# Kernel optimization log

Measured on AMD Instinct MI355X. Metric: run time of the kernel, lower is better.

Reference implementation:

```python
import jax, jax.numpy as jnp
import numpy as np

B = 512       # batch
D = 256       # n_embd
NH = 4        # heads
NN = 8 * D // NH   # neurons per head = 512
NTOT = NH * NN     # 2048
DH = D // NH       # 64
K = 8              # thinking steps
EPS_LN = 1e-5


def _ln(x, g, b):
    mu = jnp.mean(x, axis=-1, keepdims=True)
    var = jnp.mean((x - mu) ** 2, axis=-1, keepdims=True)
    return (x - mu) * jax.lax.rsqrt(var + EPS_LN) * g + b


def setup_inputs() -> dict:
    key = jax.random.key(0)
    ks = jax.random.split(key, 12)
    s = 0.02
    w = lambda k, shape: (jax.random.normal(k, shape, jnp.float32) * s)
    return {
        "boards": jax.random.normal(ks[0], (B, 12, 8, 8), jnp.float32),
        # board_encoder: Linear(768,d) -> GELU -> LN(d) -> Linear(d,d); weights stored (in,out)
        "enc_w1": w(ks[1], (768, D)), "enc_b1": jnp.zeros((D,), jnp.float32),
        "enc_ln_g": jnp.ones((D,), jnp.float32), "enc_ln_b": jnp.zeros((D,), jnp.float32),
        "enc_w2": w(ks[2], (D, D)), "enc_b2": jnp.zeros((D,), jnp.float32),
        "xinit_w": w(ks[3], (D, NTOT)), "xinit_b": jnp.zeros((NTOT,), jnp.float32),
        "D_y": w(ks[4], (NH, D, NN)),
        "E": w(ks[5], (NTOT, D)),
        "D_x": w(ks[6], (NH, D, NN)),
        "By_w": w(ks[7], (D, D)),
        "Bx_w": w(ks[8], (D, D)),
        "lna_g": jnp.ones((D,), jnp.float32), "lna_b": jnp.zeros((D,), jnp.float32),
        "lnz_g": jnp.ones((D,), jnp.float32), "lnz_b": jnp.zeros((D,), jnp.float32),
        "log_damping": jnp.asarray(np.log(0.9 / 0.1), jnp.float32),
        "vh_w1": w(ks[9], (D, D // 2)), "vh_b1": jnp.zeros((D // 2,), jnp.float32),
        "vh_w2": w(ks[10], (D // 2, 1)), "vh_b2": jnp.zeros((1,), jnp.float32),
    }


def reference(boards, enc_w1, enc_b1, enc_ln_g, enc_ln_b, enc_w2, enc_b2,
              xinit_w, xinit_b, D_y, E, D_x, By_w, Bx_w,
              lna_g, lna_b, lnz_g, lnz_b, log_damping,
              vh_w1, vh_b1, vh_w2, vh_b2):
    Bn = boards.shape[0]
    flat = boards.reshape(Bn, 768)
    h = jax.nn.gelu(flat @ enc_w1 + enc_b1, approximate=False)
    h = _ln(h, enc_ln_g, enc_ln_b)
    b = h @ enc_w2 + enc_b2                      # (B, d)
    x0 = jax.nn.relu(b @ xinit_w + xinit_b)      # (B, n)
    rho0 = jnp.zeros((Bn, NH, NN, DH), boards.dtype)
    lam = jax.nn.sigmoid(log_damping)
    b_y = b @ By_w
    b_x = b @ Bx_w

    def step(carry, _):
        x, rho = carry
        x_h = x.reshape(Bn, NH, NN)
        a = jnp.einsum('bhnd,bhn->bhd', rho, x_h).reshape(Bn, D)   # read from scratchpad
        a_cond = _ln(a + b_y, lna_g, lna_b)
        g = jax.nn.relu(jnp.einsum('bd,hdn->bhn', a_cond, D_y))
        y = (g * x_h).reshape(Bn, NTOT)
        z = _ln(y @ E, lnz_g, lnz_b)
        dx = jax.nn.relu(jnp.einsum('bd,hdn->bhn', z + b_x, D_x))
        x_new = x + dx.reshape(Bn, NTOT)
        xh = x_new.reshape(Bn, NH, NN)
        x_write = xh / (jnp.linalg.norm(xh, axis=-1, keepdims=True) + 1e-8)
        z_h = z.reshape(Bn, NH, DH)
        rho_new = lam * rho + (1.0 - lam) * jnp.einsum('bhn,bhd->bhnd', x_write, z_h)
        return (x_new, rho_new), z

    (_, _), zs = jax.lax.scan(step, (x0, rho0), None, length=K)
    z_last = zs[-1]                              # (B, d) from final thinking step
    v = jnp.tanh(jax.nn.gelu(z_last @ vh_w1 + vh_b1, approximate=False) @ vh_w2 + vh_b2)
    return v                                     # (B, 1)
```

## Files before the change

### kernel.cpp

```cpp
#include <hip/hip_runtime.h>
#include <hip/hip_bf16.h>
#include <math.h>

#define B_ 512
#define D_ 256
#define NH_ 4
#define NN_ 512
#define NTOT_ 2048
#define DH_ 64
#define KSTEPS 8

typedef __attribute__((ext_vector_type(8))) short bf16x8;
typedef __attribute__((ext_vector_type(4))) float f32x4;

#if __has_builtin(__builtin_amdgcn_global_load_lds)
#define HAVE_GLL 1
#else
#define HAVE_GLL 0
#endif

__device__ __forceinline__ float gelu_exact(float x) {
  return 0.5f * x * (1.0f + erff(x * 0.70710678118654752f));
}

__device__ __forceinline__ unsigned short f2b(float f) {
  union { float f; unsigned int u; } x; x.f = f;
  unsigned int u = x.u;
  unsigned int r = (u + 0x7FFFu + ((u >> 16) & 1u)) >> 16;
  return (unsigned short)r;
}

__device__ __forceinline__ float blockReduceSum256(float v, float* red) {
  int t = threadIdx.x;
  red[t] = v; __syncthreads();
  #pragma unroll
  for (int st = 128; st > 0; st >>= 1) {
    if (t < st) red[t] += red[t + st];
    __syncthreads();
  }
  float r = red[0];
  __syncthreads();
  return r;
}

#if HAVE_GLL
__device__ __forceinline__ void load16_lds(const unsigned short* g, unsigned short* l) {
  __builtin_amdgcn_global_load_lds(
      (const __attribute__((address_space(1))) unsigned int*)g,
      (__attribute__((address_space(3))) unsigned int*)l, 16, 0, 0);
}
#endif

template<int EPI>
__global__ __launch_bounds__(512) void k_gemm_x(
    const unsigned short* __restrict__ A, const unsigned short* __restrict__ W,
    const float* __restrict__ bias, float* __restrict__ xio)
{
  __shared__ __align__(16) unsigned short As[2 * 4096];
  __shared__ __align__(16) unsigned short Ws[2 * 4096];
  const int t = threadIdx.x;
  const int lane = t & 63, w = t >> 6;
  const int lr = lane & 15, lk = lane >> 4;
  const int l3 = lane >> 3, cch = lane & 7;
  const int n0 = blockIdx.x * 64, m0 = blockIdx.y * 64;
  const int wm = w & 3, wn = w >> 2;

  f32x4 acc[2];
  acc[0] = (f32x4){0.f, 0.f, 0.f, 0.f};
  acc[1] = (f32x4){0.f, 0.f, 0.f, 0.f};

#if HAVE_GLL
  #define STGX(tt) {                                                              \
      int buf_ = (tt) & 1; int kk_ = (tt) * 64;                                   \
      int r_ = w * 8 + l3;                                                        \
      load16_lds(&A[(size_t)(m0 + r_) * 256 + kk_ + ((cch ^ (r_ & 7)) << 3)],     \
                 &As[buf_ * 4096 + w * 512]);                                     \
      load16_lds(&W[(size_t)(n0 + r_) * 256 + kk_ + ((cch ^ (r_ & 7)) << 3)],     \
                 &Ws[buf_ * 4096 + w * 512]); }
  STGX(0);
  for (int tt = 0; tt < 4; tt++) {
    asm volatile("s_waitcnt vmcnt(0)" ::: "memory");
    __builtin_amdgcn_s_barrier();
    asm volatile("" ::: "memory");
    if (tt + 1 < 4) STGX(tt + 1);
    const unsigned short* Ab = &As[(tt & 1) * 4096];
    const unsigned short* Wb = &Ws[(tt & 1) * 4096];
    #pragma unroll
    for (int ks = 0; ks < 2; ks++) {
      int q = ks * 4 + lk;
      int r = wm * 16 + lr;
      bf16x8 af = *(const bf16x8*)&Ab[r * 64 + ((q ^ (r & 7)) << 3)];
      #pragma unroll
      for (int j = 0; j < 2; j++) {
        int c = wn * 32 + j * 16 + lr;
        bf16x8 bf = *(const bf16x8*)&Wb[c * 64 + ((q ^ (c & 7)) << 3)];
        acc[j] = __builtin_amdgcn_mfma_f32_16x16x32_bf16(af, bf, acc[j], 0, 0, 0);
      }
    }
  }
  #undef STGX
#else
  for (int tt = 0; tt < 4; tt++) {
    int buf_ = tt & 1; int kk_ = tt * 64;
    int r_ = w * 8 + l3;
    bf16x8 va = *(const bf16x8*)&A[(size_t)(m0 + r_) * 256 + kk_ + ((cch ^ (r_ & 7)) << 3)];
    *(bf16x8*)&As[buf_ * 4096 + r_ * 64 + cch * 8] = va;
    bf16x8 vw = *(const bf16x8*)&W[(size_t)(n0 + r_) * 256 + kk_ + ((cch ^ (r_ & 7)) << 3)];
    *(bf16x8*)&Ws[buf_ * 4096 + r_ * 64 + cch * 8] = vw;
    __syncthreads();
    const unsigned short* Ab = &As[buf_ * 4096];
    const unsigned short* Wb = &Ws[buf_ * 4096];
    #pragma unroll
    for (int ks = 0; ks < 2; ks++) {
      int q = ks * 4 + lk;
      int r = wm * 16 + lr;
      bf16x8 af = *(const bf16x8*)&Ab[r * 64 + ((q ^ (r & 7)) << 3)];
      #pragma unroll
      for (int j = 0; j < 2; j++) {
        int c = wn * 32 + j * 16 + lr;
        bf16x8 bf = *(const bf16x8*)&Wb[c * 64 + ((q ^ (c & 7)) << 3)];
        acc[j] = __builtin_amdgcn_mfma_f32_16x16x32_bf16(af, bf, acc[j], 0, 0, 0);
      }
    }
    __syncthreads();
  }
#endif

  #pragma unroll
  for (int j = 0; j < 2; j++)
    #pragma unroll
    for (int qq = 0; qq < 4; qq++) {
      int r = m0 + wm * 16 + lk * 4 + qq;
      int c = n0 + wn * 32 + j * 16 + lr;
      float v = acc[j][qq];
      if (EPI == 0) v = fmaxf(v + bias[c], 0.f);
      else          v = fmaxf(v, 0.f) + xio[(size_t)r * NTOT_ + c];
      xio[(size_t)r * NTOT_ + c] = v;
    }
}

__global__ __launch_bounds__(512) void k_yz(
    const unsigned short* __restrict__ acond_bf, const unsigned short* __restrict__ DyT,
    const unsigned short* __restrict__ ET, const float* __restrict__ x,
    float* __restrict__ zparts)
{
  __shared__ __align__(16) unsigned short As[2 * 4096];
  __shared__ __align__(16) unsigned short Ws[2 * 4096];
  __shared__ __align__(16) unsigned short Es[256 * 64];
  __shared__ __align__(16) unsigned short ytile[64 * 64];
  const int t = threadIdx.x;
  const int lane = t & 63, w = t >> 6;
  const int lr = lane & 15, lk = lane >> 4;
  const int l3 = lane >> 3, cch = lane & 7;
  const int nt_ = blockIdx.x, mt = blockIdx.y;
  const int m0 = mt * 64, n0 = nt_ * 64;
  const int wm = w & 3, wn = w >> 2;

  f32x4 acc[2];
  acc[0] = (f32x4){0.f, 0.f, 0.f, 0.f};
  acc[1] = (f32x4){0.f, 0.f, 0.f, 0.f};

#if HAVE_GLL
  #define STGY(tt) {                                                                  \
      int buf_ = (tt) & 1; int kk_ = (tt) * 64;                                       \
      int r_ = w * 8 + l3;                                                            \
      load16_lds(&acond_bf[(size_t)(m0 + r_) * 256 + kk_ + ((cch ^ (r_ & 7)) << 3)],  \
                 &As[buf_ * 4096 + w * 512]);                                         \
      load16_lds(&DyT[(size_t)(n0 + r_) * 256 + kk_ + ((cch ^ (r_ & 7)) << 3)],       \
                 &Ws[buf_ * 4096 + w * 512]); }
  STGY(0);
  #pragma unroll
  for (int p = 0; p < 4; p++) {
    int d = p * 64 + w * 8 + l3;
    load16_lds(&ET[(size_t)d * 2048 + n0 + ((cch ^ (d & 7)) << 3)],
               &Es[(p * 64 + w * 8) * 64]);
  }
  for (int tt = 0; tt < 4; tt++) {
    asm volatile("s_waitcnt vmcnt(0)" ::: "memory");
    __builtin_amdgcn_s_barrier();
    asm volatile("" ::: "memory");
    if (tt + 1 < 4) STGY(tt + 1);
    const unsigned short* Ab = &As[(tt & 1) * 4096];
    const unsigned short* Wb = &Ws[(tt & 1) * 4096];
    #pragma unroll
    for (int ks = 0; ks < 2; ks++) {
      int q = ks * 4 + lk;
      int r = wm * 16 + lr;
      bf16x8 af = *(const bf16x8*)&Ab[r * 64 + ((q ^ (r & 7)) << 3)];
      #pragma unroll
      for (int j = 0; j < 2; j++) {
        int c = wn * 32 + j * 16 + lr;
        bf16x8 bf = *(const bf16x8*)&Wb[c * 64 + ((q ^ (c & 7)) << 3)];
        acc[j] = __builtin_amdgcn_mfma_f32_16x16x32_bf16(af, bf, acc[j], 0, 0, 0);
      }
    }
  }
  #undef STGY
#else
  #pragma unroll
  for (int p = 0; p < 4; p++) {
    int d = p * 64 + w * 8 + l3;
    bf16x8 ve = *(const bf16x8*)&ET[(size_t)d * 2048 + n0 + ((cch ^ (d & 7)) << 3)];
    *(bf16x8*)&Es[d * 64 + cch * 8] = ve;
  }
  for (int tt = 0; tt < 4; tt++) {
    int buf_ = tt & 1; int kk_ = tt * 64;
    int r_ = w * 8 + l3;
    bf16x8 va = *(const bf16x8*)&acond_bf[(size_t)(m0 + r_) * 256 + kk_ + ((cch ^ (r_ & 7)) << 3)];
    *(bf16x8*)&As[buf_ * 4096 + r_ * 64 + cch * 8] = va;
    bf16x8 vw = *(const bf16x8*)&DyT[(size_t)(n0 + r_) * 256 + kk_ + ((cch ^ (r_ & 7)) << 3)];
    *(bf16x8*)&Ws[buf_ * 4096 + r_ * 64 + cch * 8] = vw;
    __syncthreads();
    const unsigned short* Ab = &As[buf_ * 4096];
    const unsigned short* Wb = &Ws[buf_ * 4096];
    #pragma unroll
    for (int ks = 0; ks < 2; ks++) {
      int q = ks * 4 + lk;
      int r = wm * 16 + lr;
      bf16x8 af = *(const bf16x8*)&Ab[r * 64 + ((q ^ (r & 7)) << 3)];
      #pragma unroll
      for (int j = 0; j < 2; j++) {
        int c = wn * 32 + j * 16 + lr;
        bf16x8 bf = *(const bf16x8*)&Wb[c * 64 + ((q ^ (c & 7)) << 3)];
        acc[j] = __builtin_amdgcn_mfma_f32_16x16x32_bf16(af, bf, acc[j], 0, 0, 0);
      }
    }
    __syncthreads();
  }
#endif

  #pragma unroll
  for (int j = 0; j < 2; j++)
    #pragma unroll
    for (int qq = 0; qq < 4; qq++) {
      int rl = wm * 16 + lk * 4 + qq;
      int cl = wn * 32 + j * 16 + lr;
      float v = fmaxf(acc[j][qq], 0.f) * x[(size_t)(m0 + rl) * NTOT_ + n0 + cl];
      ytile[rl * 64 + ((((cl >> 3) ^ (rl & 7)) << 3) | (cl & 7))] = f2b(v);
    }
  __syncthreads();

  f32x4 zacc[8];
  #pragma unroll
  for (int j = 0; j < 8; j++) zacc[j] = (f32x4){0.f, 0.f, 0.f, 0.f};
  #pragma unroll
  for (int ks = 0; ks < 2; ks++) {
    int q = ks * 4 + lk;
    int r = wm * 16 + lr;
    bf16x8 af = *(const bf16x8*)&ytile[r * 64 + ((q ^ (r & 7)) << 3)];
    #pragma unroll
    for (int j = 0; j < 8; j++) {
      int c = wn * 128 + j * 16 + lr;
      bf16x8 bf = *(const bf16x8*)&Es[c * 64 + ((q ^ (c & 7)) << 3)];
      zacc[j] = __builtin_amdgcn_mfma_f32_16x16x32_bf16(af, bf, zacc[j], 0, 0, 0);
    }
  }
  float* zp = zparts + (size_t)nt_ * (B_ * D_);
  #pragma unroll
  for (int j = 0; j < 8; j++)
    #pragma unroll
    for (int qq = 0; qq < 4; qq++) {
      int r = m0 + wm * 16 + lk * 4 + qq;
      int d = wn * 128 + j * 16 + lr;
      zp[(size_t)r * D_ + d] = zacc[j][qq];
    }
}

template<int ACT>
__global__ __launch_bounds__(256) void gemm_tile(
    const float* __restrict__ A, const float* __restrict__ W,
    const float* __restrict__ bias, float* __restrict__ out,
    unsigned short* __restrict__ outb, int M, int N, int K, int kchunk)
{
  __shared__ float As[16][68];
  __shared__ float Bs[16][68];
  const int tid = threadIdx.x;
  const int row0 = blockIdx.y * 64;
  const int col0 = blockIdx.x * 64;
  const int k0 = blockIdx.z * kchunk;
  const int ty = tid >> 4, tx = tid & 15;
  const int ar = tid >> 4, ak = tid & 15;
  const int br = tid >> 6, bc = tid & 63;
  float acc[4][4] = {};
  for (int kk = k0; kk < k0 + kchunk; kk += 16) {
    #pragma unroll
    for (int i = 0; i < 4; i++) {
      int r = ar + i * 16;
      As[ak][r] = A[(size_t)(row0 + r) * K + kk + ak];
    }
    #pragma unroll
    for (int i = 0; i < 4; i++) {
      int kr = br + i * 4;
      Bs[kr][bc] = W[(size_t)(kk + kr) * N + col0 + bc];
    }
    __syncthreads();
    #pragma unroll
    for (int q = 0; q < 16; q++) {
      float4 av = *(const float4*)&As[q][ty * 4];
      float4 bv = *(const float4*)&Bs[q][tx * 4];
      float aa[4] = {av.x, av.y, av.z, av.w};
      float bb[4] = {bv.x, bv.y, bv.z, bv.w};
      #pragma unroll
      for (int i = 0; i < 4; i++)
        #pragma unroll
        for (int j = 0; j < 4; j++)
          acc[i][j] = fmaf(aa[i], bb[j], acc[i][j]);
    }
    __syncthreads();
  }
  const bool parts = (gridDim.z > 1);
  float* o = out + (parts ? (size_t)blockIdx.z * (size_t)M * N : (size_t)0);
  #pragma unroll
  for (int i = 0; i < 4; i++) {
    int r = row0 + ty * 4 + i;
    #pragma unroll
    for (int j = 0; j < 4; j++) {
      int c = col0 + tx * 4 + j;
      float v = acc[i][j];
      if (!parts) {
        if (bias) v += bias[c];
        if (ACT == 2) v = gelu_exact(v);
      }
      o[(size_t)r * N + c] = v;
      if (!parts && outb) outb[(size_t)r * N + c] = f2b(v);
    }
  }
}

__global__ __launch_bounds__(256) void k_prep(
    const float* __restrict__ D_y, const float* __restrict__ D_x,
    const float* __restrict__ xinit_w, const float* __restrict__ E,
    const float* __restrict__ By_w, const float* __restrict__ Bx_w,
    unsigned short* __restrict__ DyT, unsigned short* __restrict__ DxT,
    unsigned short* __restrict__ xinitT, unsigned short* __restrict__ ET,
    float* __restrict__ Wcat)
{
  const int t = threadIdx.x;
  if (blockIdx.y == 4) {
    if (blockIdx.x >= 32) return;
    int k0 = ((int)blockIdx.x >> 3) * 64, n0 = ((int)blockIdx.x & 7) * 64;
    for (int i = 0; i < 16; i++) {
      int local = i * 256 + t;
      int kk = local >> 6, nn = local & 63;
      int n = n0 + nn;
      float v = (n < 256) ? By_w[(size_t)(k0 + kk) * 256 + n]
                          : Bx_w[(size_t)(k0 + kk) * 256 + (n - 256)];
      Wcat[(size_t)(k0 + kk) * 512 + n] = v;
    }
    return;
  }
  __shared__ float T[64][65];
  const float* in; unsigned short* out; int Kd, Nd, head, nx;
  switch (blockIdx.y) {
    case 0:  in = D_y;     out = DyT;    Kd = 256;  Nd = 2048; head = 1; nx = 32; break;
    case 1:  in = D_x;     out = DxT;    Kd = 256;  Nd = 2048; head = 1; nx = 32; break;
    case 2:  in = xinit_w; out = xinitT; Kd = 256;  Nd = 2048; head = 0; nx = 32; break;
    default: in = E;       out = ET;     Kd = 2048; Nd = 256;  head = 0; nx = 4;  break;
  }
  const int n0 = ((int)blockIdx.x % nx) * 64, k0 = ((int)blockIdx.x / nx) * 64;
  const int tx = t & 63, ty = t >> 6;
  #pragma unroll
  for (int i = 0; i < 16; i++) {
    int k = k0 + ty + i * 4;
    int n = n0 + tx;
    float v;
    if (head) v = in[((size_t)(n >> 9) * 256 + k) * 512 + (n & 511)];
    else      v = in[(size_t)k * Nd + n];
    T[ty + i * 4][tx] = v;
  }
  __syncthreads();
  #pragma unroll
  for (int i = 0; i < 16; i++) {
    int n = n0 + ty + i * 4;
    out[(size_t)n * Kd + k0 + tx] = f2b(T[tx][ty + i * 4]);
  }
}

__global__ __launch_bounds__(256) void k_ln_enc(
    const float* __restrict__ in, int nparts, int stride,
    const float* __restrict__ pre_bias,
    const float* __restrict__ g, const float* __restrict__ bta,
    float* __restrict__ out)
{
  __shared__ float red[256];
  int b = blockIdx.x, d = threadIdx.x;
  float v = 0.f;
  for (int p = 0; p < nparts; p++) v += in[(size_t)p * stride + (size_t)b * 256 + d];
  v = gelu_exact(v + pre_bias[d]);
  float mu = blockReduceSum256(v, red) * (1.f / 256.f);
  float c = v - mu;
  float var = blockReduceSum256(c * c, red) * (1.f / 256.f);
  out[(size_t)b * 256 + d] = c * rsqrtf(var + 1e-5f) * g[d] + bta[d];
}

template<int VAL>
__global__ __launch_bounds__(256) void k_ln_z(
    const float* __restrict__ zparts, const float* __restrict__ bybx,
    const float* __restrict__ lnz_g, const float* __restrict__ lnz_b,
    float* __restrict__ zh_k, unsigned short* __restrict__ zbx_bf,
    const float* __restrict__ w1, const float* __restrict__ b1,
    const float* __restrict__ w2, const float* __restrict__ b2,
    float* __restrict__ vout)
{
  __shared__ float red[256];
  __shared__ float zn[256];
  int b = blockIdx.x, d = threadIdx.x;
  float v = 0.f;
  #pragma unroll
  for (int p = 0; p < 32; p++) v += zparts[(size_t)p * (B_ * D_) + (size_t)b * D_ + d];
  float mu = blockReduceSum256(v, red) * (1.f / 256.f);
  float c = v - mu;
  float var = blockReduceSum256(c * c, red) * (1.f / 256.f);
  float vn = c * rsqrtf(var + 1e-5f) * lnz_g[d] + lnz_b[d];
  zh_k[(size_t)b * D_ + d] = vn;
  zbx_bf[(size_t)b * D_ + d] = f2b(vn + bybx[(size_t)b * 512 + 256 + d]);
  if (VAL) {
    zn[d] = vn; __syncthreads();
    int j = d & 127, ih = d >> 7;
    float s = 0.f;
    #pragma unroll 4
    for (int i = ih * 128; i < ih * 128 + 128; i++) s += zn[i] * w1[(size_t)i * 128 + j];
    red[d] = s; __syncthreads();
    if (d < 128) red[d] = gelu_exact(red[d] + red[d + 128] + b1[j]) * w2[d];
    __syncthreads();
    #pragma unroll
    for (int st = 64; st > 0; st >>= 1) {
      if (d < st) red[d] += red[d + st];
      __syncthreads();
    }
    if (d == 0) vout[b] = tanhf(red[0] + b2[0]);
  }
}

__global__ __launch_bounds__(256) void k_step_a(
    const float* __restrict__ x, float* __restrict__ xw_hist,
    const float* __restrict__ z_hist, const float* __restrict__ bybx,
    const float* __restrict__ lna_g, const float* __restrict__ lna_b,
    const float* __restrict__ log_damp, int k, unsigned short* __restrict__ out)
{
  __shared__ float dots[KSTEPS][NH_];
  __shared__ float red[256];
  int b = blockIdx.x, t = threadIdx.x;
  int lane = t & 63, wv = t >> 6;
  float lam = 1.f / (1.f + expf(-log_damp[0]));
  const float* xb = x + (size_t)b * NTOT_;
  float xv[8];
  #pragma unroll
  for (int i = 0; i < 8; i++) xv[i] = xb[t * 8 + i];

  if (k >= 1) {
    float s = 0.f;
    #pragma unroll
    for (int i = 0; i < 8; i++) s += xv[i] * xv[i];
    #pragma unroll
    for (int m = 1; m < 64; m <<= 1) s += __shfl_xor(s, m, 64);
    float inv = 1.f / (sqrtf(s) + 1e-8f);
    float* xwo = xw_hist + ((size_t)(k - 1) * B_ + b) * NTOT_;
    #pragma unroll
    for (int i = 0; i < 8; i++) xwo[t * 8 + i] = xv[i] * inv;
    if (lane == 0) dots[k - 1][wv] = s * inv;
  }
  for (int j = 0; j < k - 1; j++) {
    const float* xwb = xw_hist + ((size_t)j * B_ + b) * NTOT_;
    float s = 0.f;
    #pragma unroll
    for (int i = 0; i < 8; i++) s += xv[i] * xwb[t * 8 + i];
    #pragma unroll
    for (int off = 32; off > 0; off >>= 1) s += __shfl_down(s, off, 64);
    if (lane == 0) dots[j][wv] = s;
  }
  __syncthreads();

  int d = t;
  float av = 0.f, lp = 1.f;
  for (int j = k - 1; j >= 0; j--) {
    av += (1.f - lam) * lp * dots[j][d >> 6] * z_hist[((size_t)j * B_ + b) * D_ + d];
    lp *= lam;
  }
  av += bybx[(size_t)b * 512 + d];
  float mu = blockReduceSum256(av, red) * (1.f / 256.f);
  float c = av - mu;
  float var = blockReduceSum256(c * c, red) * (1.f / 256.f);
  out[(size_t)b * D_ + d] = f2b(c * rsqrtf(var + 1e-5f) * lna_g[d] + lna_b[d]);
}

extern "C" void kernel_launch(void* const* d_in, const int* in_sizes, int n_in,
                              void* d_out, int out_size, void* d_ws, size_t ws_size,
                              hipStream_t stream) {
  const float* boards   = (const float*)d_in[0];
  const float* enc_w1   = (const float*)d_in[1];
  const float* enc_b1   = (const float*)d_in[2];
  const float* enc_ln_g = (const float*)d_in[3];
  const float* enc_ln_b = (const float*)d_in[4];
  const float* enc_w2   = (const float*)d_in[5];
  const float* enc_b2   = (const float*)d_in[6];
  const float* xinit_w  = (const float*)d_in[7];
  const float* xinit_b  = (const float*)d_in[8];
  const float* D_y      = (const float*)d_in[9];
  const float* E        = (const float*)d_in[10];
  const float* D_x      = (const float*)d_in[11];
  const float* By_w     = (const float*)d_in[12];
  const float* Bx_w     = (const float*)d_in[13];
  const float* lna_g    = (const float*)d_in[14];
  const float* lna_b    = (const float*)d_in[15];
  const float* lnz_g    = (const float*)d_in[16];
  const float* lnz_b    = (const float*)d_in[17];
  const float* log_damp = (const float*)d_in[18];
  const float* vh_w1    = (const float*)d_in[19];
  const float* vh_b1    = (const float*)d_in[20];
  const float* vh_w2    = (const float*)d_in[21];
  const float* vh_b2    = (const float*)d_in[22];
  float* outp = (float*)d_out;

  float* ws = (float*)d_ws;
  size_t o = 0;
  float* x      = ws + o; o += (size_t)B_ * NTOT_;
  float* xw     = ws + o; o += (size_t)KSTEPS * B_ * NTOT_;
  float* zh     = ws + o; o += (size_t)KSTEPS * B_ * D_;
  float* hparts = ws + o; o += (size_t)8 * B_ * D_;
  float* h      = ws + o; o += (size_t)B_ * D_;
  float* bvec   = ws + o; o += (size_t)B_ * D_;
  float* bybx   = ws + o; o += (size_t)B_ * 512;
  float* Wcat   = ws + o; o += (size_t)256 * 512;
  float* zparts = ws + o; o += (size_t)32 * B_ * D_;
  unsigned short* DyT     = (unsigned short*)(ws + o); o += (size_t)NTOT_ * D_ / 2;
  unsigned short* DxT     = (unsigned short*)(ws + o); o += (size_t)NTOT_ * D_ / 2;
  unsigned short* ET      = (unsigned short*)(ws + o); o += (size_t)D_ * NTOT_ / 2;
  unsigned short* xinitT  = (unsigned short*)(ws + o); o += (size_t)NTOT_ * D_ / 2;
  unsigned short* bvec_bf = (unsigned short*)(ws + o); o += (size_t)B_ * D_ / 2;
  unsigned short* acond_bf= (unsigned short*)(ws + o); o += (size_t)B_ * D_ / 2;
  unsigned short* zbx_bf  = (unsigned short*)(ws + o); o += (size_t)B_ * D_ / 2;

  k_prep<<<dim3(128, 5), 256, 0, stream>>>(D_y, D_x, xinit_w, E, By_w, Bx_w,
                                           DyT, DxT, xinitT, ET, Wcat);
  gemm_tile<0><<<dim3(4, 8, 8), 256, 0, stream>>>(boards, enc_w1, nullptr, hparts,
                                                  nullptr, B_, D_, 768, 96);
  k_ln_enc<<<B_, 256, 0, stream>>>(hparts, 8, B_ * D_, enc_b1, enc_ln_g, enc_ln_b, h);
  gemm_tile<0><<<dim3(4, 8, 1), 256, 0, stream>>>(h, enc_w2, enc_b2, bvec, bvec_bf,
                                                  B_, D_, D_, D_);
  gemm_tile<0><<<dim3(8, 8, 1), 256, 0, stream>>>(bvec, Wcat, nullptr, bybx, nullptr,
                                                  B_, 512, D_, D_);
  k_gemm_x<0><<<dim3(32, 8), 512, 0, stream>>>(bvec_bf, xinitT, xinit_b, x);

  for (int k = 0; k < KSTEPS; k++) {
    k_step_a<<<B_, 256, 0, stream>>>(x, xw, zh, bybx, lna_g, lna_b, log_damp, k, acond_bf);
    k_yz<<<dim3(32, 8), 512, 0, stream>>>(acond_bf, DyT, ET, x, zparts);
    if (k < KSTEPS - 1) {
      k_ln_z<0><<<B_, 256, 0, stream>>>(zparts, bybx, lnz_g, lnz_b,
                                        zh + (size_t)k * B_ * D_, zbx_bf,
                                        nullptr, nullptr, nullptr, nullptr, nullptr);
      k_gemm_x<1><<<dim3(32, 8), 512, 0, stream>>>(zbx_bf, DxT, nullptr, x);
    } else {
      k_ln_z<1><<<B_, 256, 0, stream>>>(zparts, bybx, lnz_g, lnz_b,
                                        zh + (size_t)k * B_ * D_, zbx_bf,
                                        vh_w1, vh_b1, vh_w2, vh_b2, outp);
    }
  }
}
```

Baseline: 389.0 us.

## Fuse scratchpad read and LayerNorm into k_yz, compute dots in gemm_x epilogue

Removes the per-step k_step_a kernel. The x·xw history dot products and per-head norms are now accumulated with atomics in the k_gemm_x epilogue, and k_yz rebuilds a_cond (decayed sum of z history plus b_y, then LayerNorm) directly into LDS before the D_y GEMM. k_yz also writes the normalized xw rows and zeroes the double-buffered dot and norm buffers. This saves one launch per step and the acond_bf round trip through global memory. In exchange it adds atomics, redundant a_cond computation in every n-tile block (32x), and extra LDS use.

```diff
diff --git a/kernel.cpp b/kernel.cpp
--- a/kernel.cpp
+++ b/kernel.cpp
@@ -4,10 +4,7 @@
 
 #define B_ 512
 #define D_ 256
-#define NH_ 4
-#define NN_ 512
 #define NTOT_ 2048
-#define DH_ 64
 #define KSTEPS 8
 
 typedef __attribute__((ext_vector_type(8))) short bf16x8;
@@ -43,18 +40,34 @@
   return r;
 }
 
+__device__ __forceinline__ float red8(float v) {
+  v += __shfl_xor(v, 1, 64); v += __shfl_xor(v, 2, 64); v += __shfl_xor(v, 4, 64);
+  return v;
+}
+
 #if HAVE_GLL
-__device__ __forceinline__ void load16_lds(const unsigned short* g, unsigned short* l) {
+__device__ __forceinline__ void stage16(const unsigned short* g, unsigned short* base, int lane) {
+  (void)lane;
   __builtin_amdgcn_global_load_lds(
       (const __attribute__((address_space(1))) unsigned int*)g,
-      (__attribute__((address_space(3))) unsigned int*)l, 16, 0, 0);
-}
+      (__attribute__((address_space(3))) unsigned int*)base, 16, 0, 0);
+}
+#define WAITV0 asm volatile("s_waitcnt vmcnt(0)" ::: "memory")
+#else
+__device__ __forceinline__ void stage16(const unsigned short* g, unsigned short* base, int lane) {
+  *(bf16x8*)(base + lane * 8) = *(const bf16x8*)g;
+}
+#define WAITV0 asm volatile("s_waitcnt vmcnt(0) lgkmcnt(0)" ::: "memory")
 #endif
 
-template<int EPI>
+#define BAR() { __builtin_amdgcn_s_barrier(); asm volatile("" ::: "memory"); }
+
+template<int EPI, int DOTS>
 __global__ __launch_bounds__(512) void k_gemm_x(
     const unsigned short* __restrict__ A, const unsigned short* __restrict__ W,
-    const float* __restrict__ bias, float* __restrict__ xio)
+    const float* __restrict__ bias, float* __restrict__ xio,
+    const float* __restrict__ xw, float* __restrict__ dotbuf,
+    float* __restrict__ normbuf, int k)
 {
   __shared__ __align__(16) unsigned short As[2 * 4096];
   __shared__ __align__(16) unsigned short Ws[2 * 4096];
@@ -69,19 +82,17 @@
   acc[0] = (f32x4){0.f, 0.f, 0.f, 0.f};
   acc[1] = (f32x4){0.f, 0.f, 0.f, 0.f};
 
-#if HAVE_GLL
   #define STGX(tt) {                                                              \
       int buf_ = (tt) & 1; int kk_ = (tt) * 64;                                   \
       int r_ = w * 8 + l3;                                                        \
-      load16_lds(&A[(size_t)(m0 + r_) * 256 + kk_ + ((cch ^ (r_ & 7)) << 3)],     \
-                 &As[buf_ * 4096 + w * 512]);                                     \
-      load16_lds(&W[(size_t)(n0 + r_) * 256 + kk_ + ((cch ^ (r_ & 7)) << 3)],     \
-                 &Ws[buf_ * 4096 + w * 512]); }
+      stage16(&A[(size_t)(m0 + r_) * 256 + kk_ + ((cch ^ (r_ & 7)) << 3)],        \
+              &As[buf_ * 4096 + w * 512], lane);                                  \
+      stage16(&W[(size_t)(n0 + r_) * 256 + kk_ + ((cch ^ (r_ & 7)) << 3)],        \
+              &Ws[buf_ * 4096 + w * 512], lane); }
   STGX(0);
   for (int tt = 0; tt < 4; tt++) {
-    asm volatile("s_waitcnt vmcnt(0)" ::: "memory");
-    __builtin_amdgcn_s_barrier();
-    asm volatile("" ::: "memory");
+    WAITV0;
+    BAR();
     if (tt + 1 < 4) STGX(tt + 1);
     const unsigned short* Ab = &As[(tt & 1) * 4096];
     const unsigned short* Wb = &Ws[(tt & 1) * 4096];
@@ -97,35 +108,11 @@
         acc[j] = __builtin_amdgcn_mfma_f32_16x16x32_bf16(af, bf, acc[j], 0, 0, 0);
       }
     }
+    BAR();
   }
   #undef STGX
-#else
-  for (int tt = 0; tt < 4; tt++) {
-    int buf_ = tt & 1; int kk_ = tt * 64;
-    int r_ = w * 8 + l3;
-    bf16x8 va = *(const bf16x8*)&A[(size_t)(m0 + r_) * 256 + kk_ + ((cch ^ (r_ & 7)) << 3)];
-    *(bf16x8*)&As[buf_ * 4096 + r_ * 64 + cch * 8] = va;
-    bf16x8 vw = *(const bf16x8*)&W[(size_t)(n0 + r_) * 256 + kk_ + ((cch ^ (r_ & 7)) << 3)];
-    *(bf16x8*)&Ws[buf_ * 4096 + r_ * 64 + cch * 8] = vw;
-    __syncthreads();
-    const unsigned short* Ab = &As[buf_ * 4096];
-    const unsigned short* Wb = &Ws[buf_ * 4096];
-    #pragma unroll
-    for (int ks = 0; ks < 2; ks++) {
-      int q = ks * 4 + lk;
-      int r = wm * 16 + lr;
-      bf16x8 af = *(const bf16x8*)&Ab[r * 64 + ((q ^ (r & 7)) << 3)];
-      #pragma unroll
-      for (int j = 0; j < 2; j++) {
-        int c = wn * 32 + j * 16 + lr;
-        bf16x8 bf = *(const bf16x8*)&Wb[c * 64 + ((q ^ (c & 7)) << 3)];
-        acc[j] = __builtin_amdgcn_mfma_f32_16x16x32_bf16(af, bf, acc[j], 0, 0, 0);
-      }
-    }
-    __syncthreads();
-  }
-#endif
-
+
+  float vout[2][4];
   #pragma unroll
   for (int j = 0; j < 2; j++)
     #pragma unroll
@@ -136,107 +123,176 @@
       if (EPI == 0) v = fmaxf(v + bias[c], 0.f);
       else          v = fmaxf(v, 0.f) + xio[(size_t)r * NTOT_ + c];
       xio[(size_t)r * NTOT_ + c] = v;
-    }
+      vout[j][qq] = v;
+    }
+
+  if (DOTS) {
+    __syncthreads();
+    float* xfl = (float*)&As[0];
+    #pragma unroll
+    for (int j = 0; j < 2; j++)
+      #pragma unroll
+      for (int qq = 0; qq < 4; qq++)
+        xfl[(wm * 16 + lk * 4 + qq) * 64 + wn * 32 + j * 16 + lr] = vout[j][qq];
+    __syncthreads();
+    const int row = t >> 3, sub = t & 7;
+    const int gr = m0 + row;
+    const int headx = n0 >> 9;
+    const int p = k & 1;
+    float xv8[8]; float nrm = 0.f;
+    #pragma unroll
+    for (int e = 0; e < 8; e++) {
+      xv8[e] = xfl[row * 64 + sub * 8 + e];
+      nrm += xv8[e] * xv8[e];
+    }
+    nrm = red8(nrm);
+    if (sub == 0) atomicAdd(&normbuf[(p * 512 + gr) * 4 + headx], nrm);
+    for (int j = 0; j < k; j++) {
+      const float* wr = &xw[((size_t)j * B_ + gr) * NTOT_ + n0 + sub * 8];
+      float s = 0.f;
+      #pragma unroll
+      for (int e = 0; e < 8; e++) s += xv8[e] * wr[e];
+      s = red8(s);
+      if (sub == 0) atomicAdd(&dotbuf[((p * 7 + j) * 512 + gr) * 4 + headx], s);
+    }
+  }
 }
 
 __global__ __launch_bounds__(512) void k_yz(
-    const unsigned short* __restrict__ acond_bf, const unsigned short* __restrict__ DyT,
-    const unsigned short* __restrict__ ET, const float* __restrict__ x,
-    float* __restrict__ zparts)
+    const unsigned short* __restrict__ DyT, const unsigned short* __restrict__ ET,
+    const float* __restrict__ x, const float* __restrict__ bybx,
+    const float* __restrict__ zhg,
+    const float* __restrict__ lna_g, const float* __restrict__ lna_b,
+    const float* __restrict__ log_damp,
+    float* __restrict__ xw, float* __restrict__ dotbuf, float* __restrict__ normbuf,
+    float* __restrict__ zparts, int k)
 {
-  __shared__ __align__(16) unsigned short As[2 * 4096];
-  __shared__ __align__(16) unsigned short Ws[2 * 4096];
+  __shared__ __align__(16) unsigned short Abuf[4][4096];
+  __shared__ __align__(16) unsigned short Dys[4][4096];
   __shared__ __align__(16) unsigned short Es[256 * 64];
-  __shared__ __align__(16) unsigned short ytile[64 * 64];
+  __shared__ __align__(16) unsigned short ytile[4096];
+  __shared__ float invn_s[64];
   const int t = threadIdx.x;
   const int lane = t & 63, w = t >> 6;
   const int lr = lane & 15, lk = lane >> 4;
   const int l3 = lane >> 3, cch = lane & 7;
-  const int nt_ = blockIdx.x, mt = blockIdx.y;
-  const int m0 = mt * 64, n0 = nt_ * 64;
+  const int nt = blockIdx.x, mt = blockIdx.y;
+  const int m0 = mt * 64, n0 = nt * 64;
   const int wm = w & 3, wn = w >> 2;
-
-  f32x4 acc[2];
-  acc[0] = (f32x4){0.f, 0.f, 0.f, 0.f};
-  acc[1] = (f32x4){0.f, 0.f, 0.f, 0.f};
-
-#if HAVE_GLL
-  #define STGY(tt) {                                                                  \
-      int buf_ = (tt) & 1; int kk_ = (tt) * 64;                                       \
-      int r_ = w * 8 + l3;                                                            \
-      load16_lds(&acond_bf[(size_t)(m0 + r_) * 256 + kk_ + ((cch ^ (r_ & 7)) << 3)],  \
-                 &As[buf_ * 4096 + w * 512]);                                         \
-      load16_lds(&DyT[(size_t)(n0 + r_) * 256 + kk_ + ((cch ^ (r_ & 7)) << 3)],       \
-                 &Ws[buf_ * 4096 + w * 512]); }
-  STGY(0);
+  const int qb = (k - 1) & 1, pz = k & 1;
+
+  #pragma unroll
+  for (int kt = 0; kt < 4; kt++) {
+    int rr = w * 8 + l3;
+    stage16(&DyT[(size_t)(n0 + rr) * 256 + kt * 64 + ((cch ^ (rr & 7)) << 3)],
+            &Dys[kt][w * 512], lane);
+  }
   #pragma unroll
   for (int p = 0; p < 4; p++) {
     int d = p * 64 + w * 8 + l3;
-    load16_lds(&ET[(size_t)d * 2048 + n0 + ((cch ^ (d & 7)) << 3)],
-               &Es[(p * 64 + w * 8) * 64]);
-  }
-  for (int tt = 0; tt < 4; tt++) {
-    asm volatile("s_waitcnt vmcnt(0)" ::: "memory");
-    __builtin_amdgcn_s_barrier();
-    asm volatile("" ::: "memory");
-    if (tt + 1 < 4) STGY(tt + 1);
-    const unsigned short* Ab = &As[(tt & 1) * 4096];
-    const unsigned short* Wb = &Ws[(tt & 1) * 4096];
+    stage16(&ET[(size_t)d * 2048 + n0 + ((cch ^ (d & 7)) << 3)],
+            &Es[(p * 64 + w * 8) * 64], lane);
+  }
+
+  {
+    const float lam = 1.f / (1.f + expf(-log_damp[0]));
+    const int row = t >> 3, sub = t & 7;
+    const int gr = m0 + row;
+    const int head = sub >> 1;
+    float a8[32];
+    #pragma unroll
+    for (int i = 0; i < 32; i++) a8[i] = 0.f;
+    if (k >= 1) {
+      float nb = normbuf[(qb * 512 + gr) * 4 + head];
+      if (sub == 0) {
+        float nx = normbuf[(qb * 512 + gr) * 4 + (n0 >> 9)];
+        invn_s[row] = 1.f / (sqrtf(nx) + 1e-8f);
+      }
+      float lp = 1.f;
+      for (int j = k - 1; j >= 0; j--) {
+        float djv = (j == k - 1) ? nb / (sqrtf(nb) + 1e-8f)
+                                 : dotbuf[((qb * 7 + j) * 512 + gr) * 4 + head];
+        float cj = (1.f - lam) * lp * djv;
+        const float* zr = zhg + ((size_t)j * B_ + gr) * D_ + sub * 32;
+        #pragma unroll
+        for (int i8 = 0; i8 < 8; i8++) {
+          float4 zv = *(const float4*)(zr + i8 * 4);
+          a8[i8 * 4 + 0] += cj * zv.x; a8[i8 * 4 + 1] += cj * zv.y;
+          a8[i8 * 4 + 2] += cj * zv.z; a8[i8 * 4 + 3] += cj * zv.w;
+        }
+        lp *= lam;
+      }
+    }
+    const float* byr = bybx + (size_t)gr * 512 + sub * 32;
+    #pragma unroll
+    for (int i8 = 0; i8 < 8; i8++) {
+      float4 bv = *(const float4*)(byr + i8 * 4);
+      a8[i8 * 4 + 0] += bv.x; a8[i8 * 4 + 1] += bv.y;
+      a8[i8 * 4 + 2] += bv.z; a8[i8 * 4 + 3] += bv.w;
+    }
+    float s = 0.f;
+    #pragma unroll
+    for (int i = 0; i < 32; i++) s += a8[i];
+    s = red8(s);
+    float mu = s * (1.f / 256.f);
+    float s2 = 0.f;
+    #pragma unroll
+    for (int i = 0; i < 32; i++) { float cc = a8[i] - mu; s2 += cc * cc; }
+    s2 = red8(s2);
+    float rin = rsqrtf(s2 * (1.f / 256.f) + 1e-5f);
+    int kt = sub >> 1;
+    #pragma unroll
+    for (int cc4 = 0; cc4 < 4; cc4++) {
+      int c64 = (sub & 1) * 4 + cc4;
+      bf16x8 pk;
+      #pragma unroll
+      for (int e = 0; e < 8; e++) {
+        int d = sub * 32 + cc4 * 8 + e;
+        pk[e] = (short)f2b((a8[cc4 * 8 + e] - mu) * rin * lna_g[d] + lna_b[d]);
+      }
+      *(bf16x8*)&Abuf[kt][row * 64 + ((c64 ^ (row & 7)) << 3)] = pk;
+    }
+  }
+  if (nt == 0) {
+    for (int idx = t; idx < 7 * 64 * 4; idx += 512) {
+      int j = idx >> 8, rem = idx & 255;
+      dotbuf[((pz * 7 + j) * 512 + m0 + (rem >> 2)) * 4 + (rem & 3)] = 0.f;
+    }
+    if (t < 256) normbuf[(pz * 512 + m0 + (t >> 2)) * 4 + (t & 3)] = 0.f;
+  }
+
+  WAITV0;
+  __syncthreads();
+
+  f32x4 yacc[2];
+  yacc[0] = (f32x4){0.f, 0.f, 0.f, 0.f};
+  yacc[1] = (f32x4){0.f, 0.f, 0.f, 0.f};
+  #pragma unroll
+  for (int kt = 0; kt < 4; kt++)
     #pragma unroll
     for (int ks = 0; ks < 2; ks++) {
       int q = ks * 4 + lk;
       int r = wm * 16 + lr;
-      bf16x8 af = *(const bf16x8*)&Ab[r * 64 + ((q ^ (r & 7)) << 3)];
+      bf16x8 af = *(const bf16x8*)&Abuf[kt][r * 64 + ((q ^ (r & 7)) << 3)];
       #pragma unroll
-      for (int j = 0; j < 2; j++) {
-        int c = wn * 32 + j * 16 + lr;
-        bf16x8 bf = *(const bf16x8*)&Wb[c * 64 + ((q ^ (c & 7)) << 3)];
-        acc[j] = __builtin_amdgcn_mfma_f32_16x16x32_bf16(af, bf, acc[j], 0, 0, 0);
+      for (int j2 = 0; j2 < 2; j2++) {
+        int c = wn * 32 + j2 * 16 + lr;
+        bf16x8 bf = *(const bf16x8*)&Dys[kt][c * 64 + ((q ^ (c & 7)) << 3)];
+        yacc[j2] = __builtin_amdgcn_mfma_f32_16x16x32_bf16(af, bf, yacc[j2], 0, 0, 0);
       }
     }
-  }
-  #undef STGY
-#else
-  #pragma unroll
-  for (int p = 0; p < 4; p++) {
-    int d = p * 64 + w * 8 + l3;
-    bf16x8 ve = *(const bf16x8*)&ET[(size_t)d * 2048 + n0 + ((cch ^ (d & 7)) << 3)];
-    *(bf16x8*)&Es[d * 64 + cch * 8] = ve;
-  }
-  for (int tt = 0; tt < 4; tt++) {
-    int buf_ = tt & 1; int kk_ = tt * 64;
-    int r_ = w * 8 + l3;
-    bf16x8 va = *(const bf16x8*)&acond_bf[(size_t)(m0 + r_) * 256 + kk_ + ((cch ^ (r_ & 7)) << 3)];
-    *(bf16x8*)&As[buf_ * 4096 + r_ * 64 + cch * 8] = va;
-    bf16x8 vw = *(const bf16x8*)&DyT[(size_t)(n0 + r_) * 256 + kk_ + ((cch ^ (r_ & 7)) << 3)];
-    *(bf16x8*)&Ws[buf_ * 4096 + r_ * 64 + cch * 8] = vw;
-    __syncthreads();
-    const unsigned short* Ab = &As[buf_ * 4096];
-    const unsigned short* Wb = &Ws[buf_ * 4096];
-    #pragma unroll
-    for (int ks = 0; ks < 2; ks++) {
-      int q = ks * 4 + lk;
-      int r = wm * 16 + lr;
-      bf16x8 af = *(const bf16x8*)&Ab[r * 64 + ((q ^ (r & 7)) << 3)];
-      #pragma unroll
-      for (int j = 0; j < 2; j++) {
-        int c = wn * 32 + j * 16 + lr;
-        bf16x8 bf = *(const bf16x8*)&Wb[c * 64 + ((q ^ (c & 7)) << 3)];
-        acc[j] = __builtin_amdgcn_mfma_f32_16x16x32_bf16(af, bf, acc[j], 0, 0, 0);
-      }
-    }
-    __syncthreads();
-  }
-#endif
-
-  #pragma unroll
-  for (int j = 0; j < 2; j++)
+  const bool wxw = (k >= 1 && k < KSTEPS - 1);
+  #pragma unroll
+  for (int j2 = 0; j2 < 2; j2++)
     #pragma unroll
     for (int qq = 0; qq < 4; qq++) {
       int rl = wm * 16 + lk * 4 + qq;
-      int cl = wn * 32 + j * 16 + lr;
-      float v = fmaxf(acc[j][qq], 0.f) * x[(size_t)(m0 + rl) * NTOT_ + n0 + cl];
+      int cl = wn * 32 + j2 * 16 + lr;
+      float xv = x[(size_t)(m0 + rl) * NTOT_ + n0 + cl];
+      float v = fmaxf(yacc[j2][qq], 0.f) * xv;
       ytile[rl * 64 + ((((cl >> 3) ^ (rl & 7)) << 3) | (cl & 7))] = f2b(v);
+      if (wxw)
+        xw[((size_t)(k - 1) * B_ + m0 + rl) * NTOT_ + n0 + cl] = xv * invn_s[rl];
     }
   __syncthreads();
 
@@ -255,7 +311,7 @@
       zacc[j] = __builtin_amdgcn_mfma_f32_16x16x32_bf16(af, bf, zacc[j], 0, 0, 0);
     }
   }
-  float* zp = zparts + (size_t)nt_ * (B_ * D_);
+  float* zp = zparts + (size_t)nt * (B_ * D_);
   #pragma unroll
   for (int j = 0; j < 8; j++)
     #pragma unroll
@@ -430,58 +486,6 @@
     }
     if (d == 0) vout[b] = tanhf(red[0] + b2[0]);
   }
-}
-
-__global__ __launch_bounds__(256) void k_step_a(
-    const float* __restrict__ x, float* __restrict__ xw_hist,
-    const float* __restrict__ z_hist, const float* __restrict__ bybx,
-    const float* __restrict__ lna_g, const float* __restrict__ lna_b,
-    const float* __restrict__ log_damp, int k, unsigned short* __restrict__ out)
-{
-  __shared__ float dots[KSTEPS][NH_];
-  __shared__ float red[256];
-  int b = blockIdx.x, t = threadIdx.x;
-  int lane = t & 63, wv = t >> 6;
-  float lam = 1.f / (1.f + expf(-log_damp[0]));
-  const float* xb = x + (size_t)b * NTOT_;
-  float xv[8];
-  #pragma unroll
-  for (int i = 0; i < 8; i++) xv[i] = xb[t * 8 + i];
-
-  if (k >= 1) {
-    float s = 0.f;
-    #pragma unroll
-    for (int i = 0; i < 8; i++) s += xv[i] * xv[i];
-    #pragma unroll
-    for (int m = 1; m < 64; m <<= 1) s += __shfl_xor(s, m, 64);
-    float inv = 1.f / (sqrtf(s) + 1e-8f);
-    float* xwo = xw_hist + ((size_t)(k - 1) * B_ + b) * NTOT_;
-    #pragma unroll
-    for (int i = 0; i < 8; i++) xwo[t * 8 + i] = xv[i] * inv;
-    if (lane == 0) dots[k - 1][wv] = s * inv;
-  }
-  for (int j = 0; j < k - 1; j++) {
-    const float* xwb = xw_hist + ((size_t)j * B_ + b) * NTOT_;
-    float s = 0.f;
-    #pragma unroll
-    for (int i = 0; i < 8; i++) s += xv[i] * xwb[t * 8 + i];
-    #pragma unroll
-    for (int off = 32; off > 0; off >>= 1) s += __shfl_down(s, off, 64);
-    if (lane == 0) dots[j][wv] = s;
-  }
-  __syncthreads();
-
-  int d = t;
-  float av = 0.f, lp = 1.f;
-  for (int j = k - 1; j >= 0; j--) {
-    av += (1.f - lam) * lp * dots[j][d >> 6] * z_hist[((size_t)j * B_ + b) * D_ + d];
-    lp *= lam;
-  }
-  av += bybx[(size_t)b * 512 + d];
-  float mu = blockReduceSum256(av, red) * (1.f / 256.f);
-  float c = av - mu;
-  float var = blockReduceSum256(c * c, red) * (1.f / 256.f);
-  out[(size_t)b * D_ + d] = f2b(c * rsqrtf(var + 1e-5f) * lna_g[d] + lna_b[d]);
 }
 
 extern "C" void kernel_launch(void* const* d_in, const int* in_sizes, int n_in,
@@ -515,7 +519,7 @@
   float* ws = (float*)d_ws;
   size_t o = 0;
   float* x      = ws + o; o += (size_t)B_ * NTOT_;
-  float* xw     = ws + o; o += (size_t)KSTEPS * B_ * NTOT_;
+  float* xw     = ws + o; o += (size_t)7 * B_ * NTOT_;
   float* zh     = ws + o; o += (size_t)KSTEPS * B_ * D_;
   float* hparts = ws + o; o += (size_t)8 * B_ * D_;
   float* h      = ws + o; o += (size_t)B_ * D_;
@@ -523,12 +527,13 @@
   float* bybx   = ws + o; o += (size_t)B_ * 512;
   float* Wcat   = ws + o; o += (size_t)256 * 512;
   float* zparts = ws + o; o += (size_t)32 * B_ * D_;
+  float* dotbuf = ws + o; o += (size_t)2 * 7 * 512 * 4;
+  float* normbuf= ws + o; o += (size_t)2 * 512 * 4;
   unsigned short* DyT     = (unsigned short*)(ws + o); o += (size_t)NTOT_ * D_ / 2;
   unsigned short* DxT     = (unsigned short*)(ws + o); o += (size_t)NTOT_ * D_ / 2;
   unsigned short* ET      = (unsigned short*)(ws + o); o += (size_t)D_ * NTOT_ / 2;
   unsigned short* xinitT  = (unsigned short*)(ws + o); o += (size_t)NTOT_ * D_ / 2;
   unsigned short* bvec_bf = (unsigned short*)(ws + o); o += (size_t)B_ * D_ / 2;
-  unsigned short* acond_bf= (unsigned short*)(ws + o); o += (size_t)B_ * D_ / 2;
   unsigned short* zbx_bf  = (unsigned short*)(ws + o); o += (size_t)B_ * D_ / 2;
 
   k_prep<<<dim3(128, 5), 256, 0, stream>>>(D_y, D_x, xinit_w, E, By_w, Bx_w,
@@ -540,16 +545,19 @@
                                                   B_, D_, D_, D_);
   gemm_tile<0><<<dim3(8, 8, 1), 256, 0, stream>>>(bvec, Wcat, nullptr, bybx, nullptr,
                                                   B_, 512, D_, D_);
-  k_gemm_x<0><<<dim3(32, 8), 512, 0, stream>>>(bvec_bf, xinitT, xinit_b, x);
+  k_gemm_x<0, 0><<<dim3(32, 8), 512, 0, stream>>>(bvec_bf, xinitT, xinit_b, x,
+                                                  nullptr, nullptr, nullptr, 0);
 
   for (int k = 0; k < KSTEPS; k++) {
-    k_step_a<<<B_, 256, 0, stream>>>(x, xw, zh, bybx, lna_g, lna_b, log_damp, k, acond_bf);
-    k_yz<<<dim3(32, 8), 512, 0, stream>>>(acond_bf, DyT, ET, x, zparts);
+    k_yz<<<dim3(32, 8), 512, 0, stream>>>(DyT, ET, x, bybx, zh,
+                                          lna_g, lna_b, log_damp,
+                                          xw, dotbuf, normbuf, zparts, k);
     if (k < KSTEPS - 1) {
       k_ln_z<0><<<B_, 256, 0, stream>>>(zparts, bybx, lnz_g, lnz_b,
                                         zh + (size_t)k * B_ * D_, zbx_bf,
                                         nullptr, nullptr, nullptr, nullptr, nullptr);
-      k_gemm_x<1><<<dim3(32, 8), 512, 0, stream>>>(zbx_bf, DxT, nullptr, x);
+      k_gemm_x<1, 1><<<dim3(32, 8), 512, 0, stream>>>(zbx_bf, DxT, nullptr, x,
+                                                      xw, dotbuf, normbuf, k);
     } else {
       k_ln_z<1><<<B_, 256, 0, stream>>>(zparts, bybx, lnz_g, lnz_b,
                                         zh + (size_t)k * B_ * D_, zbx_bf,
```

New measurement: 433.2 us. 11.4% more time.
